# Kernel tuning notes

Hardware: AMD Instinct MI355X
Metric: run time of the kernel (lower is better)

Reference implementation:

```python
import jax, jax.numpy as jnp
import numpy as np

EPS = 1e-6
H = 16  # heads

def rmsnorm(x, w):
    return x * jax.lax.rsqrt(jnp.mean(x * x, axis=-1, keepdims=True) + EPS) * w

def l2norm(x):
    return x * jax.lax.rsqrt(jnp.sum(x * x, axis=-1, keepdims=True) + EPS)

def setup_inputs() -> dict:
    key = jax.random.key(0)
    ks = jax.random.split(key, 12)
    B, S, D, F = 2, 2048, 1024, 4096
    std = 0.02
    inp = {
        'hidden_states': jax.random.normal(ks[0], (B, S, D), jnp.float32),
        'Wq': jax.random.normal(ks[1], (D, D), jnp.float32) * std,
        'Wk': jax.random.normal(ks[2], (D, D), jnp.float32) * std,
        'Wv': jax.random.normal(ks[3], (D, D), jnp.float32) * std,
        'Wb': jax.random.normal(ks[4], (D, H), jnp.float32) * std,
        'Wo': jax.random.normal(ks[5], (D, D), jnp.float32) * std,
        'ln1': jnp.ones((D,), jnp.float32),
        'ln2': jnp.ones((D,), jnp.float32),
        'Wg': jax.random.normal(ks[6], (D, F), jnp.float32) * std,
        'Wu': jax.random.normal(ks[7], (D, F), jnp.float32) * std,
        'Wd': jax.random.normal(ks[8], (F, D), jnp.float32) * std,
    }
    return inp

def delta_rule(q, k, v, beta):
    # q,k: [B,S,H,dk] (l2-normalized), v: [B,S,H,dv], beta: [B,S,H]
    B, S, Hh, dk = q.shape
    dv = v.shape[-1]
    # time-major for scan: [S,B,H,...]
    qt = jnp.moveaxis(q, 1, 0)
    kt = jnp.moveaxis(k, 1, 0)
    vt = jnp.moveaxis(v, 1, 0)
    bt = jnp.moveaxis(beta, 1, 0)

    def step(Sm, inp):
        qi, ki, vi, bi = inp  # [B,H,dk],[B,H,dk],[B,H,dv],[B,H]
        Sk = jnp.einsum('bhkv,bhk->bhv', Sm, ki)          # S^T k
        upd = ki[..., :, None] * (vi - Sk)[..., None, :]  # outer(k, v - S^T k)
        Sm = Sm + bi[..., None, None] * upd
        oi = jnp.einsum('bhkv,bhk->bhv', Sm, qi)
        return Sm, oi

    S0 = jnp.zeros((B, Hh, dk, dv), q.dtype)
    _, out = jax.lax.scan(step, S0, (qt, kt, vt, bt))
    return jnp.moveaxis(out, 0, 1)  # [B,S,H,dv]

def reference(hidden_states, Wq, Wk, Wv, Wb, Wo, ln1, ln2, Wg, Wu, Wd):
    B, S, D = hidden_states.shape
    dk = D // H
    # --- delta-rule attention sub-block ---
    x = rmsnorm(hidden_states, ln1)
    q = l2norm(jax.nn.silu(x @ Wq).reshape(B, S, H, dk))
    k = l2norm(jax.nn.silu(x @ Wk).reshape(B, S, H, dk))
    v = jax.nn.silu(x @ Wv).reshape(B, S, H, dk)
    beta = jax.nn.sigmoid(x @ Wb)  # [B,S,H]
    o = delta_rule(q, k, v, beta).reshape(B, S, D)
    h = hidden_states + o @ Wo
    # --- SwiGLU MLP sub-block ---
    y = rmsnorm(h, ln2)
    h = h + (jax.nn.silu(y @ Wg) * (y @ Wu)) @ Wd
    return h
```

## Files before the change

kernel.cpp:

```cpp
#include <hip/hip_runtime.h>
#include <hip/hip_bf16.h>
#include <stdint.h>

#define BB 2
#define SS 2048
#define DD 1024
#define FF 4096
#define HH 16
#define ROWS (BB*SS)
#define NC 32
#define NQKV 3200

typedef float f32x4 __attribute__((ext_vector_type(4)));
typedef __bf16 bf16x8 __attribute__((ext_vector_type(8)));

typedef __attribute__((address_space(1))) const void* gas1p;
typedef __attribute__((address_space(3))) void* las3p;

__device__ __forceinline__ void gload16(const void* g, void* l) {
    __builtin_amdgcn_global_load_lds((gas1p)g, (las3p)l, 16, 0, 0);
}

__device__ __forceinline__ unsigned short f2bf(float f) {
    unsigned int u = __builtin_bit_cast(unsigned int, f);
    u += 0x7fffu + ((u >> 16) & 1u);
    return (unsigned short)(u >> 16);
}
__device__ __forceinline__ float bf2f(unsigned short s) {
    unsigned int u = ((unsigned int)s) << 16;
    return __builtin_bit_cast(float, u);
}
__device__ __forceinline__ float sigmoidf_(float x) { return 1.f / (1.f + __expf(-x)); }
__device__ __forceinline__ float siluf_(float x)    { return x / (1.f + __expf(-x)); }

__device__ __forceinline__ int swz(int b) { return b ^ (((b >> 7) & 7) << 4); }

__device__ __forceinline__ void tp_body(const float* __restrict__ W,
                                        unsigned short* __restrict__ Wt,
                                        int K, int N, int bx, int by, int tid) {
    __shared__ float tile[32][33];
    int tx = tid & 31, ty = tid >> 5;
    int n0 = bx * 32, k0 = by * 32;
#pragma unroll
    for (int i = 0; i < 4; ++i)
        tile[ty + 8 * i][tx] = W[(size_t)(k0 + ty + 8 * i) * N + n0 + tx];
    __syncthreads();
#pragma unroll
    for (int i = 0; i < 4; ++i)
        Wt[(size_t)(n0 + ty + 8 * i) * K + k0 + tx] = f2bf(tile[tx][ty + 8 * i]);
}

__global__ __launch_bounds__(256) void transpose_cvt(const float* __restrict__ W,
                                                     unsigned short* __restrict__ Wt,
                                                     int K, int N) {
    tp_body(W, Wt, K, N, blockIdx.x, blockIdx.y, threadIdx.x);
}

__global__ __launch_bounds__(256) void transpose_cvt4(const float* W0, const float* W1,
                                                      const float* W2, const float* W3,
                                                      unsigned short* T0, unsigned short* T1,
                                                      unsigned short* T2, unsigned short* T3) {
    const float* W = (blockIdx.z == 0) ? W0 : (blockIdx.z == 1) ? W1 : (blockIdx.z == 2) ? W2 : W3;
    unsigned short* T = (blockIdx.z == 0) ? T0 : (blockIdx.z == 1) ? T1 : (blockIdx.z == 2) ? T2 : T3;
    tp_body(W, T, DD, DD, blockIdx.x, blockIdx.y, threadIdx.x);
}

__global__ __launch_bounds__(256) void transpose_cvt2(const float* W0, const float* W1,
                                                      unsigned short* T0, unsigned short* T1) {
    const float* W = (blockIdx.z == 0) ? W0 : W1;
    unsigned short* T = (blockIdx.z == 0) ? T0 : T1;
    tp_body(W, T, DD, FF, blockIdx.x, blockIdx.y, threadIdx.x);
}

__global__ __launch_bounds__(256) void wbt_kernel(const float* __restrict__ Wb,
                                                  unsigned short* __restrict__ WbT) {
    int idx = blockIdx.x * 256 + threadIdx.x;
    int d = idx >> 4, h = idx & 15;
    WbT[h * DD + d] = f2bf(Wb[idx]);
}

__global__ __launch_bounds__(256) void rmsnorm_bf16_kernel(const float* __restrict__ src,
                                                           const float* __restrict__ w,
                                                           unsigned short* __restrict__ dst) {
    int row = blockIdx.x;
    int tid = threadIdx.x;
    float4 x = ((const float4*)(src + (size_t)row * DD))[tid];
    float ss = x.x * x.x + x.y * x.y + x.z * x.z + x.w * x.w;
#pragma unroll
    for (int m = 1; m < 64; m <<= 1) ss += __shfl_xor(ss, m, 64);
    __shared__ float ws4[4];
    if ((tid & 63) == 0) ws4[tid >> 6] = ss;
    __syncthreads();
    ss = ws4[0] + ws4[1] + ws4[2] + ws4[3];
    float sc = rsqrtf(ss * (1.f / DD) + 1e-6f);
    float4 wv = ((const float4*)w)[tid];
    ushort4 o;
    o.x = f2bf(x.x * sc * wv.x);
    o.y = f2bf(x.y * sc * wv.y);
    o.z = f2bf(x.z * sc * wv.z);
    o.w = f2bf(x.w * sc * wv.w);
    ((ushort4*)(dst + (size_t)row * DD))[tid] = o;
}

#define BM 128
#define BN 128
#define BK 32

template <int EP>
__global__ __launch_bounds__(256) void gemm_bt(const unsigned short* __restrict__ A,
                                               const unsigned short* __restrict__ Bt,
                                               const float* __restrict__ res,
                                               float* __restrict__ cf,
                                               unsigned short* __restrict__ cb,
                                               int M, int N, int K) {
    __shared__ __align__(16) char sA[BM * BK * 2];
    __shared__ __align__(16) char sB[BN * BK * 2];
    int m0 = blockIdx.y * BM, n0 = blockIdx.x * BN;
    int tid = threadIdx.x;
    int lane = tid & 63, wave = tid >> 6;
    int wm = wave >> 1, wn = wave & 1;
    f32x4 acc[4][4] = {};

    for (int k0 = 0; k0 < K; k0 += BK) {
#pragma unroll
        for (int i = 0; i < 2; ++i) {
            int c = wave * 2 + i;
            int row = c * 16 + (lane >> 2);
            int col = (lane & 3) * 8;
            gload16(A  + ((size_t)(m0 + row) * K + k0 + col), (char*)sA + c * 1024);
            gload16(Bt + ((size_t)(n0 + row) * K + k0 + col), (char*)sB + c * 1024);
        }
        __syncthreads();
        bf16x8 af[4], bfr[4];
#pragma unroll
        for (int mi = 0; mi < 4; ++mi) {
            int ar = wm * 64 + mi * 16 + (lane & 15);
            af[mi] = *(const bf16x8*)(sA + ar * 64 + (lane >> 4) * 16);
        }
#pragma unroll
        for (int ni = 0; ni < 4; ++ni) {
            int br = wn * 64 + ni * 16 + (lane & 15);
            bfr[ni] = *(const bf16x8*)(sB + br * 64 + (lane >> 4) * 16);
        }
#pragma unroll
        for (int mi = 0; mi < 4; ++mi)
#pragma unroll
            for (int ni = 0; ni < 4; ++ni)
                acc[mi][ni] = __builtin_amdgcn_mfma_f32_16x16x32_bf16(af[mi], bfr[ni], acc[mi][ni], 0, 0, 0);
        __syncthreads();
    }

    int mbase = m0 + wm * 64 + (lane >> 4) * 4;
    int nbase = n0 + wn * 64 + (lane & 15);
#pragma unroll
    for (int mi = 0; mi < 4; ++mi)
#pragma unroll
        for (int ni = 0; ni < 4; ++ni)
#pragma unroll
            for (int r = 0; r < 4; ++r) {
                int m = mbase + mi * 16 + r;
                int n = nbase + ni * 16;
                float v = acc[mi][ni][r];
                if (EP == 3) {
                    int seg = n >> 10, col = n & 1023;
                    if (seg < 3)
                        cb[(size_t)seg * ROWS * DD + (size_t)m * DD + col] = f2bf(v);
                    else if (col < 16)
                        cf[(size_t)m * HH + col] = sigmoidf_(v);
                } else {
                    if (EP == 1) v += res[(size_t)m * N + n];
                    if (EP == 2) cb[(size_t)m * N + n] = f2bf(v);
                    else         cf[(size_t)m * N + n] = v;
                }
            }
}

__global__ void silu_mul_kernel(unsigned short* __restrict__ g, const unsigned short* __restrict__ u, int n4) {
    int i = blockIdx.x * blockDim.x + threadIdx.x;
    int stride = gridDim.x * blockDim.x;
    ushort4* gp = (ushort4*)g;
    const ushort4* up = (const ushort4*)u;
    for (; i < n4; i += stride) {
        ushort4 gv = gp[i];
        ushort4 uv = up[i];
        ushort4 o;
        o.x = f2bf(siluf_(bf2f(gv.x)) * bf2f(uv.x));
        o.y = f2bf(siluf_(bf2f(gv.y)) * bf2f(uv.y));
        o.z = f2bf(siluf_(bf2f(gv.z)) * bf2f(uv.z));
        o.w = f2bf(siluf_(bf2f(gv.w)) * bf2f(uv.w));
        gp[i] = o;
    }
}


__device__ __forceinline__ bf16x8 ldsfrag(const char* mat, int row, int kt, int lane) {
    return *(const bf16x8*)(mat + swz(row * 128 + kt * 64 + (lane >> 4) * 16));
}

template <bool INIT_P>
__device__ __forceinline__ void mm64(const char* X, const char* Y, const char* P,
                                     f32x4 acc[4], int w, int lane) {
    int g = lane >> 4;
#pragma unroll
    for (int j = 0; j < 4; ++j) {
        if (INIT_P) {
#pragma unroll
            for (int r = 0; r < 4; ++r) {
                int m = 16 * w + g * 4 + r, n = (lane & 15) + 16 * j;
                acc[j][r] = bf2f(*(const unsigned short*)(P + swz(m * 128 + n * 2)));
            }
        } else {
            acc[j] = (f32x4){0.f, 0.f, 0.f, 0.f};
        }
    }
    bf16x8 xs0 = ldsfrag(X, 16 * w + (lane & 15), 0, lane);
    bf16x8 xs1 = ldsfrag(X, 16 * w + (lane & 15), 1, lane);
#pragma unroll
    for (int j = 0; j < 4; ++j) {
        bf16x8 y0 = ldsfrag(Y, 16 * j + (lane & 15), 0, lane);
        bf16x8 y1 = ldsfrag(Y, 16 * j + (lane & 15), 1, lane);
        acc[j] = __builtin_amdgcn_mfma_f32_16x16x32_bf16(xs0, y0, acc[j], 0, 0, 0);
        acc[j] = __builtin_amdgcn_mfma_f32_16x16x32_bf16(xs1, y1, acc[j], 0, 0, 0);
    }
}

__device__ __forceinline__ void wR(char* D, const f32x4 acc[4], int w, int lane, int mode) {
    int g = lane >> 4;
#pragma unroll
    for (int j = 0; j < 4; ++j)
#pragma unroll
        for (int r = 0; r < 4; ++r) {
            int m = 16 * w + g * 4 + r, n = (lane & 15) + 16 * j;
            float v = acc[j][r];
            if (mode >= 1) v = (n < m) ? v : 0.f;
            if (mode == 2) v = ((m == n) ? 1.f : 0.f) - v;
            *(unsigned short*)(D + swz(m * 128 + n * 2)) = f2bf(v);
        }
}

__device__ __forceinline__ void wT(char* D, const f32x4 acc[4], int w, int lane, int mode) {
    int g = lane >> 4;
#pragma unroll
    for (int j = 0; j < 4; ++j) {
        int n = (lane & 15) + 16 * j, m0 = 16 * w + g * 4;
        ushort4 pk;
        pk.x = (mode == 1 && !(n < m0 + 0)) ? (unsigned short)0 : f2bf(acc[j][0]);
        pk.y = (mode == 1 && !(n < m0 + 1)) ? (unsigned short)0 : f2bf(acc[j][1]);
        pk.z = (mode == 1 && !(n < m0 + 2)) ? (unsigned short)0 : f2bf(acc[j][2]);
        pk.w = (mode == 1 && !(n < m0 + 3)) ? (unsigned short)0 : f2bf(acc[j][3]);
        *(ushort4*)(D + swz(n * 128 + m0 * 2)) = pk;
    }
}

__device__ __forceinline__ void load16bf(const unsigned short* p, float* v) {
    uint4 a = *(const uint4*)p, b = *(const uint4*)(p + 8);
    unsigned int u0[8] = {a.x, a.y, a.z, a.w, b.x, b.y, b.z, b.w};
#pragma unroll
    for (int i = 0; i < 8; ++i) {
        v[2 * i]     = bf2f((unsigned short)(u0[i] & 0xffffu));
        v[2 * i + 1] = bf2f((unsigned short)(u0[i] >> 16));
    }
}

__global__ __launch_bounds__(256) void delta_prep_kernel(const unsigned short* __restrict__ qb,
                                                         const unsigned short* __restrict__ kb,
                                                         const unsigned short* __restrict__ vb,
                                                         const float* __restrict__ betab,
                                                         char* __restrict__ chunkbuf) {
    __shared__ __align__(16) char sK[8192], sKb[8192], sKbT[8192], sVbT[8192], sQ[8192];
    __shared__ __align__(16) char mA[8192], mAT[8192], mB2[8192], mBT[8192], mP0[8192], mP1[8192];

    int ci = blockIdx.x;
    int c = ci & 31, h = (ci >> 5) & 15, b = ci >> 9;
    int tid = threadIdx.x;
    int lane = tid & 63, w = tid >> 6;

    char* cbuf = chunkbuf + (size_t)ci * 40960;
    unsigned short* Qg  = (unsigned short*)(cbuf);
    unsigned short* KTg = (unsigned short*)(cbuf + 8192);
    unsigned short* Ag  = (unsigned short*)(cbuf + 16384);
    unsigned short* Wg  = (unsigned short*)(cbuf + 24576);
    unsigned short* U0g = (unsigned short*)(cbuf + 32768);

    {
        int trow = tid >> 2, part = tid & 3, d0 = part * 16;
        size_t rg = (size_t)b * SS + c * 64 + trow;
        float bet = betab[rg * HH + h];
        size_t base = rg * DD + h * 64 + d0;

        float qv[16], kv[16], vv[16];
        load16bf(qb + base, qv);
        load16bf(kb + base, kv);
        load16bf(vb + base, vv);

        float ssq = 0.f, ssk = 0.f;
#pragma unroll
        for (int i = 0; i < 16; ++i) {
            qv[i] = siluf_(qv[i]); ssq += qv[i] * qv[i];
            kv[i] = siluf_(kv[i]); ssk += kv[i] * kv[i];
            vv[i] = siluf_(vv[i]);
        }
        ssq += __shfl_xor(ssq, 1, 64); ssq += __shfl_xor(ssq, 2, 64);
        ssk += __shfl_xor(ssk, 1, 64); ssk += __shfl_xor(ssk, 2, 64);
        float scq = rsqrtf(ssq + 1e-6f), sck = rsqrtf(ssk + 1e-6f);
#pragma unroll
        for (int i = 0; i < 16; ++i) { qv[i] *= scq; kv[i] *= sck; }

#pragma unroll
        for (int m = 0; m < 4; ++m) {
            ushort4 pq, pk_, pkb;
#pragma unroll
            for (int r = 0; r < 4; ++r) {
                ((unsigned short*)&pq)[r]  = f2bf(qv[4 * m + r]);
                ((unsigned short*)&pk_)[r] = f2bf(kv[4 * m + r]);
                ((unsigned short*)&pkb)[r] = f2bf(bet * kv[4 * m + r]);
            }
            int bo = trow * 128 + (d0 + 4 * m) * 2;
            *(ushort4*)(sQ + swz(bo))  = pq;
            *(ushort4*)(sK + swz(bo))  = pk_;
            *(ushort4*)(sKb + swz(bo)) = pkb;
            *(ushort4*)(Qg + trow * 64 + d0 + 4 * m) = pq;
        }
#pragma unroll
        for (int e = 0; e < 16; ++e) {
            int d = d0 + e;
            *(unsigned short*)(sKbT + swz(d * 128 + trow * 2)) = f2bf(bet * kv[e]);
            *(unsigned short*)(sVbT + swz(d * 128 + trow * 2)) = f2bf(bet * vv[e]);
            KTg[d * 64 + trow] = f2bf(kv[e]);
        }
    }
    __syncthreads();

    f32x4 acc[4];
    mm64<false>(sKb, sK, nullptr, acc, w, lane);
    wR(mA, acc, w, lane, 1);
    wT(mAT, acc, w, lane, 1);
    wR(mP0, acc, w, lane, 2);
    __syncthreads();

    char *cX = mA, *cXT = mAT, *nX = mB2, *nXT = mBT, *pc = mP0, *pn = mP1;
#pragma unroll
    for (int s = 0; s < 5; ++s) {
        mm64<false>(cX, cXT, nullptr, acc, w, lane);
        wR(nX, acc, w, lane, 0);
        wT(nXT, acc, w, lane, 0);
        __syncthreads();
        mm64<true>(pc, nXT, pc, acc, w, lane);
        wR(pn, acc, w, lane, 0);
        __syncthreads();
        char* t;
        t = cX; cX = nX; nX = t;
        t = cXT; cXT = nXT; nXT = t;
        t = pc; pc = pn; pn = t;
    }

    int g = lane >> 4;
    mm64<false>(sK, sQ, nullptr, acc, w, lane);
#pragma unroll
    for (int j = 0; j < 4; ++j) {
        int n = (lane & 15) + 16 * j, m0 = 16 * w + g * 4;
        ushort4 pk;
        pk.x = (m0 + 0 <= n) ? f2bf(acc[j][0]) : (unsigned short)0;
        pk.y = (m0 + 1 <= n) ? f2bf(acc[j][1]) : (unsigned short)0;
        pk.z = (m0 + 2 <= n) ? f2bf(acc[j][2]) : (unsigned short)0;
        pk.w = (m0 + 3 <= n) ? f2bf(acc[j][3]) : (unsigned short)0;
        *(ushort4*)(Ag + n * 64 + m0) = pk;
    }
    mm64<false>(sKbT, pc, nullptr, acc, w, lane);
#pragma unroll
    for (int j = 0; j < 4; ++j) {
        int n = (lane & 15) + 16 * j, m0 = 16 * w + g * 4;
        ushort4 pk;
        pk.x = f2bf(acc[j][0]); pk.y = f2bf(acc[j][1]);
        pk.z = f2bf(acc[j][2]); pk.w = f2bf(acc[j][3]);
        *(ushort4*)(Wg + n * 64 + m0) = pk;
    }
    mm64<false>(pc, sVbT, nullptr, acc, w, lane);
#pragma unroll
    for (int j = 0; j < 4; ++j) {
        int n = (lane & 15) + 16 * j, m0 = 16 * w + g * 4;
        ushort4 pk;
        pk.x = f2bf(acc[j][0]); pk.y = f2bf(acc[j][1]);
        pk.z = f2bf(acc[j][2]); pk.w = f2bf(acc[j][3]);
        *(ushort4*)(U0g + n * 64 + m0) = pk;
    }
}

__global__ __launch_bounds__(256) void delta_seq_kernel(const char* __restrict__ chunkbuf,
                                                        unsigned short* __restrict__ ob) {
    __shared__ __align__(16) char stg[2 * 40960 + 8192 + 8192];
    int bh = blockIdx.x;
    int b = bh >> 4, h = bh & 15;
    int tid = threadIdx.x;
    int lane = tid & 63, w = tid >> 6, g = lane >> 4;

    char* UTw = stg + 81920 + w * 2048;
    char* Slw = stg + 90112 + w * 2048;

    f32x4 s_acc[4];
#pragma unroll
    for (int j = 0; j < 4; ++j) s_acc[j] = (f32x4){0.f, 0.f, 0.f, 0.f};
    uint4 z4 = {0, 0, 0, 0};
    *(uint4*)(Slw + lane * 32) = z4;
    *(uint4*)(Slw + lane * 32 + 16) = z4;

    const char* cbase = chunkbuf + (size_t)bh * NC * 40960;
    int lo = (lane * 16) ^ ((lane >> 3) << 4);
    int pw = 10 * w;

    {
        const char* src = cbase;
        char* dst = stg;
#pragma unroll
        for (int p = 0; p < 10; ++p)
            gload16(src + (pw + p) * 1024 + lo, dst + (pw + p) * 1024);
    }

    for (int c = 0; c < NC; ++c) {
        {
            const char* src = cbase + (size_t)((c + 1) & 31) * 40960;
            char* dst = stg + ((c + 1) & 1) * 40960;
#pragma unroll
            for (int p = 0; p < 10; ++p)
                gload16(src + (pw + p) * 1024 + lo, dst + (pw + p) * 1024);
        }
        asm volatile("s_waitcnt vmcnt(10)" ::: "memory");
        __builtin_amdgcn_s_barrier();
        __builtin_amdgcn_sched_barrier(0);

        const char* cur = stg + (c & 1) * 40960;
        const char* Qm = cur, *KTm = cur + 8192, *Am = cur + 16384, *Wm = cur + 24576, *U0m = cur + 32768;

        bf16x8 xs0 = ldsfrag(Slw, lane & 15, 0, lane);
        bf16x8 xs1 = ldsfrag(Slw, lane & 15, 1, lane);

        f32x4 ut[4];
        f32x4 oa[4];
#pragma unroll
        for (int j = 0; j < 4; ++j) { ut[j] = (f32x4){0.f, 0.f, 0.f, 0.f}; oa[j] = (f32x4){0.f, 0.f, 0.f, 0.f}; }
#pragma unroll
        for (int j = 0; j < 4; ++j) {
            bf16x8 y0 = ldsfrag(Wm, 16 * j + (lane & 15), 0, lane);
            bf16x8 y1 = ldsfrag(Wm, 16 * j + (lane & 15), 1, lane);
            ut[j] = __builtin_amdgcn_mfma_f32_16x16x32_bf16(xs0, y0, ut[j], 0, 0, 0);
            ut[j] = __builtin_amdgcn_mfma_f32_16x16x32_bf16(xs1, y1, ut[j], 0, 0, 0);
        }
#pragma unroll
        for (int j = 0; j < 4; ++j) {
            bf16x8 y0 = ldsfrag(Qm, 16 * j + (lane & 15), 0, lane);
            bf16x8 y1 = ldsfrag(Qm, 16 * j + (lane & 15), 1, lane);
            oa[j] = __builtin_amdgcn_mfma_f32_16x16x32_bf16(xs0, y0, oa[j], 0, 0, 0);
            oa[j] = __builtin_amdgcn_mfma_f32_16x16x32_bf16(xs1, y1, oa[j], 0, 0, 0);
        }
#pragma unroll
        for (int j = 0; j < 4; ++j)
#pragma unroll
            for (int r = 0; r < 4; ++r) {
                int m = 16 * w + g * 4 + r;
                int n = (lane & 15) + 16 * j;
                float u0 = bf2f(*(const unsigned short*)(U0m + swz(m * 128 + n * 2)));
                float u = u0 - ut[j][r];
                *(unsigned short*)(UTw + swz((g * 4 + r) * 128 + n * 2)) = f2bf(u);
            }
        bf16x8 us0 = ldsfrag(UTw, lane & 15, 0, lane);
        bf16x8 us1 = ldsfrag(UTw, lane & 15, 1, lane);
#pragma unroll
        for (int j = 0; j < 4; ++j) {
            bf16x8 y0 = ldsfrag(Am, 16 * j + (lane & 15), 0, lane);
            bf16x8 y1 = ldsfrag(Am, 16 * j + (lane & 15), 1, lane);
            oa[j] = __builtin_amdgcn_mfma_f32_16x16x32_bf16(us0, y0, oa[j], 0, 0, 0);
            oa[j] = __builtin_amdgcn_mfma_f32_16x16x32_bf16(us1, y1, oa[j], 0, 0, 0);
        }
#pragma unroll
        for (int j = 0; j < 4; ++j) {
            bf16x8 y0 = ldsfrag(KTm, 16 * j + (lane & 15), 0, lane);
            bf16x8 y1 = ldsfrag(KTm, 16 * j + (lane & 15), 1, lane);
            s_acc[j] = __builtin_amdgcn_mfma_f32_16x16x32_bf16(us0, y0, s_acc[j], 0, 0, 0);
            s_acc[j] = __builtin_amdgcn_mfma_f32_16x16x32_bf16(us1, y1, s_acc[j], 0, 0, 0);
        }
#pragma unroll
        for (int j = 0; j < 4; ++j) {
            int n = (lane & 15) + 16 * j;
            size_t tg = (size_t)b * SS + c * 64 + n;
            int col = h * 64 + 16 * w + g * 4;
            ushort4 pk;
            pk.x = f2bf(oa[j][0]); pk.y = f2bf(oa[j][1]);
            pk.z = f2bf(oa[j][2]); pk.w = f2bf(oa[j][3]);
            *(ushort4*)(ob + tg * DD + col) = pk;
        }
#pragma unroll
        for (int j = 0; j < 4; ++j)
#pragma unroll
            for (int r = 0; r < 4; ++r) {
                int n = (lane & 15) + 16 * j;
                *(unsigned short*)(Slw + swz((g * 4 + r) * 128 + n * 2)) = f2bf(s_acc[j][r]);
            }

        asm volatile("" ::: "memory");
        __builtin_amdgcn_s_barrier();
        __builtin_amdgcn_sched_barrier(0);
    }
}

extern "C" void kernel_launch(void* const* d_in, const int* in_sizes, int n_in,
                              void* d_out, int out_size, void* d_ws, size_t ws_size,
                              hipStream_t stream) {
    const float* hidden = (const float*)d_in[0];
    const float* Wq  = (const float*)d_in[1];
    const float* Wk  = (const float*)d_in[2];
    const float* Wv  = (const float*)d_in[3];
    const float* Wb  = (const float*)d_in[4];
    const float* Wo  = (const float*)d_in[5];
    const float* ln1 = (const float*)d_in[6];
    const float* ln2 = (const float*)d_in[7];
    const float* Wg  = (const float*)d_in[8];
    const float* Wu  = (const float*)d_in[9];
    const float* Wd  = (const float*)d_in[10];
    float* out = (float*)d_out;
    char* ws = (char*)d_ws;

    const size_t MB = 1024 * 1024;
    const size_t KB256 = 262144;
    unsigned short* wq_t = (unsigned short*)(ws + 0 * MB);
    unsigned short* wk_t = (unsigned short*)(ws + 2 * MB);
    unsigned short* wv_t = (unsigned short*)(ws + 4 * MB);
    unsigned short* wbT  = (unsigned short*)(ws + 6 * MB);
    unsigned short* wo_t = (unsigned short*)(ws + 6 * MB + KB256);
    unsigned short* wg_t = (unsigned short*)(ws + 8 * MB + KB256);
    unsigned short* wu_t = (unsigned short*)(ws + 16 * MB + KB256);
    unsigned short* wd_t = (unsigned short*)(ws + 24 * MB + KB256);
    float* hbuf          = (float*)(ws + 32 * MB + KB256);
    unsigned short* yb   = (unsigned short*)(ws + 48 * MB + KB256);
    unsigned short* qb   = (unsigned short*)(ws + 56 * MB + KB256);
    unsigned short* kb   = (unsigned short*)(ws + 64 * MB + KB256);
    unsigned short* vb   = (unsigned short*)(ws + 72 * MB + KB256);
    float* betab         = (float*)(ws + 80 * MB + KB256);
    unsigned short* xb   = (unsigned short*)(ws + 80 * MB + 2 * KB256);
    unsigned short* ob   = xb;
    char* chunkbuf       = ws + 88 * MB + 2 * KB256;
    unsigned short* gb = (unsigned short*)(ws + 56 * MB + KB256);
    unsigned short* ub = (unsigned short*)(ws + 88 * MB + 2 * KB256);

    dim3 blk(256);

    transpose_cvt4<<<dim3(32, 32, 4), blk, 0, stream>>>(Wq, Wk, Wv, Wo, wq_t, wk_t, wv_t, wo_t);
    transpose_cvt2<<<dim3(128, 32, 2), blk, 0, stream>>>(Wg, Wu, wg_t, wu_t);
    transpose_cvt<<<dim3(32, 128), blk, 0, stream>>>(Wd, wd_t, FF, DD);
    wbt_kernel<<<64, blk, 0, stream>>>(Wb, wbT);

    rmsnorm_bf16_kernel<<<ROWS, blk, 0, stream>>>(hidden, ln1, xb);

    gemm_bt<3><<<dim3(NQKV / BN, ROWS / BM), blk, 0, stream>>>(xb, wq_t, nullptr, betab, qb, ROWS, NQKV, DD);

    delta_prep_kernel<<<1024, blk, 0, stream>>>(qb, kb, vb, betab, chunkbuf);
    delta_seq_kernel<<<BB * HH, blk, 0, stream>>>(chunkbuf, ob);

    gemm_bt<1><<<dim3(DD / BN, ROWS / BM), blk, 0, stream>>>(ob, wo_t, hidden, hbuf, nullptr, ROWS, DD, DD);

    rmsnorm_bf16_kernel<<<ROWS, blk, 0, stream>>>(hbuf, ln2, yb);

    gemm_bt<2><<<dim3(FF / BN, ROWS / BM), blk, 0, stream>>>(yb, wg_t, nullptr, nullptr, gb, ROWS, FF, DD);
    gemm_bt<2><<<dim3(FF / BN, ROWS / BM), blk, 0, stream>>>(yb, wu_t, nullptr, nullptr, ub, ROWS, FF, DD);

    silu_mul_kernel<<<4096, blk, 0, stream>>>(gb, ub, ROWS * FF / 4);

    gemm_bt<1><<<dim3(DD / BN, ROWS / BM), blk, 0, stream>>>(gb, wd_t, hbuf, out, nullptr, ROWS, DD, FF);
}
```

Baseline: 555.0 us.

## Fuse gate/up GEMMs with SwiGLU epilogue and double-buffer GEMM with XCD-aware tiling

The Wg and Wu weights are transposed into one interleaved matrix, so a single 256x256-tile GEMM computes gate and up columns side by side and applies silu(g)*u in its epilogue. This removes the separate silu_mul kernel and the write and read-back of both intermediate bf16 buffers. The GEMM is rewritten with BK=64, double-buffered LDS staging, and a block-index remap that groups tiles by XCD for better L2 locality. The large tile uses more LDS and registers, which may lower occupancy.

Result: faster. 464.2 us (-16.4%).

```diff
diff --git a/kernel.cpp b/kernel.cpp
--- a/kernel.cpp
+++ b/kernel.cpp
@@ -65,11 +65,24 @@
     tp_body(W, T, DD, DD, blockIdx.x, blockIdx.y, threadIdx.x);
 }
 
-__global__ __launch_bounds__(256) void transpose_cvt2(const float* W0, const float* W1,
-                                                      unsigned short* T0, unsigned short* T1) {
+__global__ __launch_bounds__(256) void transpose_cvt_gu(const float* W0, const float* W1,
+                                                        unsigned short* Wt) {
     const float* W = (blockIdx.z == 0) ? W0 : W1;
-    unsigned short* T = (blockIdx.z == 0) ? T0 : T1;
-    tp_body(W, T, DD, FF, blockIdx.x, blockIdx.y, threadIdx.x);
+    int isU = blockIdx.z;
+    __shared__ float tile[32][33];
+    int tid = threadIdx.x;
+    int tx = tid & 31, ty = tid >> 5;
+    int n0 = blockIdx.x * 32, k0 = blockIdx.y * 32;
+#pragma unroll
+    for (int i = 0; i < 4; ++i)
+        tile[ty + 8 * i][tx] = W[(size_t)(k0 + ty + 8 * i) * FF + n0 + tx];
+    __syncthreads();
+#pragma unroll
+    for (int i = 0; i < 4; ++i) {
+        int j = n0 + ty + 8 * i;
+        int rint = ((j >> 4) << 5) + (j & 15) + (isU << 4);
+        Wt[(size_t)rint * DD + k0 + tx] = f2bf(tile[tx][ty + 8 * i]);
+    }
 }
 
 __global__ __launch_bounds__(256) void wbt_kernel(const float* __restrict__ Wb,
@@ -102,93 +115,116 @@
     ((ushort4*)(dst + (size_t)row * DD))[tid] = o;
 }
 
-#define BM 128
-#define BN 128
-#define BK 32
-
-template <int EP>
-__global__ __launch_bounds__(256) void gemm_bt(const unsigned short* __restrict__ A,
-                                               const unsigned short* __restrict__ Bt,
-                                               const float* __restrict__ res,
-                                               float* __restrict__ cf,
-                                               unsigned short* __restrict__ cb,
-                                               int M, int N, int K) {
-    __shared__ __align__(16) char sA[BM * BK * 2];
-    __shared__ __align__(16) char sB[BN * BK * 2];
-    int m0 = blockIdx.y * BM, n0 = blockIdx.x * BN;
-    int tid = threadIdx.x;
-    int lane = tid & 63, wave = tid >> 6;
-    int wm = wave >> 1, wn = wave & 1;
-    f32x4 acc[4][4] = {};
-
-    for (int k0 = 0; k0 < K; k0 += BK) {
-#pragma unroll
-        for (int i = 0; i < 2; ++i) {
-            int c = wave * 2 + i;
-            int row = c * 16 + (lane >> 2);
-            int col = (lane & 3) * 8;
-            gload16(A  + ((size_t)(m0 + row) * K + k0 + col), (char*)sA + c * 1024);
-            gload16(Bt + ((size_t)(n0 + row) * K + k0 + col), (char*)sB + c * 1024);
-        }
-        __syncthreads();
-        bf16x8 af[4], bfr[4];
-#pragma unroll
-        for (int mi = 0; mi < 4; ++mi) {
-            int ar = wm * 64 + mi * 16 + (lane & 15);
-            af[mi] = *(const bf16x8*)(sA + ar * 64 + (lane >> 4) * 16);
-        }
-#pragma unroll
-        for (int ni = 0; ni < 4; ++ni) {
-            int br = wn * 64 + ni * 16 + (lane & 15);
-            bfr[ni] = *(const bf16x8*)(sB + br * 64 + (lane >> 4) * 16);
-        }
-#pragma unroll
-        for (int mi = 0; mi < 4; ++mi)
-#pragma unroll
-            for (int ni = 0; ni < 4; ++ni)
-                acc[mi][ni] = __builtin_amdgcn_mfma_f32_16x16x32_bf16(af[mi], bfr[ni], acc[mi][ni], 0, 0, 0);
-        __syncthreads();
-    }
-
-    int mbase = m0 + wm * 64 + (lane >> 4) * 4;
-    int nbase = n0 + wn * 64 + (lane & 15);
-#pragma unroll
-    for (int mi = 0; mi < 4; ++mi)
-#pragma unroll
-        for (int ni = 0; ni < 4; ++ni)
-#pragma unroll
-            for (int r = 0; r < 4; ++r) {
-                int m = mbase + mi * 16 + r;
-                int n = nbase + ni * 16;
-                float v = acc[mi][ni][r];
-                if (EP == 3) {
-                    int seg = n >> 10, col = n & 1023;
-                    if (seg < 3)
-                        cb[(size_t)seg * ROWS * DD + (size_t)m * DD + col] = f2bf(v);
-                    else if (col < 16)
-                        cf[(size_t)m * HH + col] = sigmoidf_(v);
-                } else {
-                    if (EP == 1) v += res[(size_t)m * N + n];
-                    if (EP == 2) cb[(size_t)m * N + n] = f2bf(v);
-                    else         cf[(size_t)m * N + n] = v;
+template <int EP, int BMt, int BNt, int WM, int WN, bool FASTM>
+__global__ __launch_bounds__(WM * WN * 64) void gemm2(const unsigned short* __restrict__ A,
+                                                      const unsigned short* __restrict__ Bt,
+                                                      const float* __restrict__ res,
+                                                      float* __restrict__ cf,
+                                                      unsigned short* __restrict__ cb,
+                                                      int M, int N, int K) {
+    constexpr int NW = WM * WN;
+    constexpr int MI = BMt / (WM * 16);
+    constexpr int NI = BNt / (WN * 16);
+    constexpr int ACH = BMt / 8 / NW;
+    constexpr int BCH = BNt / 8 / NW;
+    constexpr int ABYTES = BMt * 128;
+    constexpr int BBYTES = BNt * 128;
+    __shared__ __align__(16) char lds[2 * (ABYTES + BBYTES)];
+
+    int tid = threadIdx.x, lane = tid & 63, w = tid >> 6;
+    int wm = w / WN, wn = w % WN;
+
+    int gm = M / BMt, gn = N / BNt, nwg = gm * gn;
+    int flat = blockIdx.x;
+    int q = nwg >> 3, r8 = nwg & 7;
+    int xcd = flat & 7, loc = flat >> 3;
+    int sid = (xcd < r8 ? xcd * (q + 1) : r8 * (q + 1) + (xcd - r8) * q) + loc;
+    int midx, nidx;
+    if (FASTM) { midx = sid % gm; nidx = sid / gm; }
+    else       { nidx = sid % gn; midx = sid / gn; }
+    int m0 = midx * BMt, n0 = nidx * BNt;
+
+    auto stage = [&](int buf, int kt) {
+        char* base = (char*)lds + buf * (ABYTES + BBYTES);
+        int row8 = lane >> 3, col = (lane & 7) * 8;
+#pragma unroll
+        for (int i = 0; i < ACH; ++i) {
+            int c = w * ACH + i;
+            gload16(A + ((size_t)(m0 + c * 8 + row8) * K + kt * 64 + col), base + c * 1024);
+        }
+#pragma unroll
+        for (int i = 0; i < BCH; ++i) {
+            int c = w * BCH + i;
+            gload16(Bt + ((size_t)(n0 + c * 8 + row8) * K + kt * 64 + col), base + ABYTES + c * 1024);
+        }
+    };
+
+    f32x4 acc[MI][NI] = {};
+    int nk = K / 64;
+    stage(0, 0);
+    __syncthreads();
+    int cur = 0;
+    for (int kt = 0; kt < nk; ++kt) {
+        if (kt + 1 < nk) stage(cur ^ 1, kt + 1);
+        const char* abuf = (const char*)lds + cur * (ABYTES + BBYTES);
+        const char* bbuf = abuf + ABYTES;
+#pragma unroll
+        for (int kk = 0; kk < 2; ++kk) {
+            bf16x8 afr[MI], bfr[NI];
+#pragma unroll
+            for (int mi = 0; mi < MI; ++mi)
+                afr[mi] = *(const bf16x8*)(abuf + (wm * (MI * 16) + mi * 16 + (lane & 15)) * 128 + kk * 64 + (lane >> 4) * 16);
+#pragma unroll
+            for (int ni = 0; ni < NI; ++ni)
+                bfr[ni] = *(const bf16x8*)(bbuf + (wn * (NI * 16) + ni * 16 + (lane & 15)) * 128 + kk * 64 + (lane >> 4) * 16);
+#pragma unroll
+            for (int mi = 0; mi < MI; ++mi)
+#pragma unroll
+                for (int ni = 0; ni < NI; ++ni)
+                    acc[mi][ni] = __builtin_amdgcn_mfma_f32_16x16x32_bf16(afr[mi], bfr[ni], acc[mi][ni], 0, 0, 0);
+        }
+        if (kt + 1 < nk) {
+            __syncthreads();
+            cur ^= 1;
+        }
+    }
+
+    int mbase = m0 + wm * (MI * 16) + (lane >> 4) * 4;
+    if (EP == 4) {
+        int j0 = (n0 + wn * (NI * 16)) / 2 + (lane & 15);
+#pragma unroll
+        for (int mi = 0; mi < MI; ++mi)
+#pragma unroll
+            for (int p = 0; p < NI / 2; ++p)
+#pragma unroll
+                for (int r = 0; r < 4; ++r) {
+                    int m = mbase + mi * 16 + r;
+                    float gv = acc[mi][2 * p][r], uv = acc[mi][2 * p + 1][r];
+                    cb[(size_t)m * FF + j0 + 16 * p] = f2bf(siluf_(gv) * uv);
                 }
-            }
-}
-
-__global__ void silu_mul_kernel(unsigned short* __restrict__ g, const unsigned short* __restrict__ u, int n4) {
-    int i = blockIdx.x * blockDim.x + threadIdx.x;
-    int stride = gridDim.x * blockDim.x;
-    ushort4* gp = (ushort4*)g;
-    const ushort4* up = (const ushort4*)u;
-    for (; i < n4; i += stride) {
-        ushort4 gv = gp[i];
-        ushort4 uv = up[i];
-        ushort4 o;
-        o.x = f2bf(siluf_(bf2f(gv.x)) * bf2f(uv.x));
-        o.y = f2bf(siluf_(bf2f(gv.y)) * bf2f(uv.y));
-        o.z = f2bf(siluf_(bf2f(gv.z)) * bf2f(uv.z));
-        o.w = f2bf(siluf_(bf2f(gv.w)) * bf2f(uv.w));
-        gp[i] = o;
+    } else {
+        int nbase = n0 + wn * (NI * 16) + (lane & 15);
+#pragma unroll
+        for (int mi = 0; mi < MI; ++mi)
+#pragma unroll
+            for (int ni = 0; ni < NI; ++ni)
+#pragma unroll
+                for (int r = 0; r < 4; ++r) {
+                    int m = mbase + mi * 16 + r;
+                    int n = nbase + ni * 16;
+                    float v = acc[mi][ni][r];
+                    if (EP == 3) {
+                        int seg = n >> 10, col = n & 1023;
+                        if (seg < 3)
+                            cb[(size_t)seg * ROWS * DD + (size_t)m * DD + col] = f2bf(v);
+                        else if (col < 16)
+                            cf[(size_t)m * HH + col] = sigmoidf_(v);
+                    } else {
+                        if (EP == 1) v += res[(size_t)m * N + n];
+                        if (EP == 2) cb[(size_t)m * N + n] = f2bf(v);
+                        else         cf[(size_t)m * N + n] = v;
+                    }
+                }
     }
 }
 
@@ -526,8 +562,7 @@
     unsigned short* wv_t = (unsigned short*)(ws + 4 * MB);
     unsigned short* wbT  = (unsigned short*)(ws + 6 * MB);
     unsigned short* wo_t = (unsigned short*)(ws + 6 * MB + KB256);
-    unsigned short* wg_t = (unsigned short*)(ws + 8 * MB + KB256);
-    unsigned short* wu_t = (unsigned short*)(ws + 16 * MB + KB256);
+    unsigned short* btGU = (unsigned short*)(ws + 8 * MB + KB256);
     unsigned short* wd_t = (unsigned short*)(ws + 24 * MB + KB256);
     float* hbuf          = (float*)(ws + 32 * MB + KB256);
     unsigned short* yb   = (unsigned short*)(ws + 48 * MB + KB256);
@@ -538,31 +573,31 @@
     unsigned short* xb   = (unsigned short*)(ws + 80 * MB + 2 * KB256);
     unsigned short* ob   = xb;
     char* chunkbuf       = ws + 88 * MB + 2 * KB256;
-    unsigned short* gb = (unsigned short*)(ws + 56 * MB + KB256);
-    unsigned short* ub = (unsigned short*)(ws + 88 * MB + 2 * KB256);
+    unsigned short* act  = (unsigned short*)(ws + 56 * MB + KB256);
 
     dim3 blk(256);
 
     transpose_cvt4<<<dim3(32, 32, 4), blk, 0, stream>>>(Wq, Wk, Wv, Wo, wq_t, wk_t, wv_t, wo_t);
-    transpose_cvt2<<<dim3(128, 32, 2), blk, 0, stream>>>(Wg, Wu, wg_t, wu_t);
+    transpose_cvt_gu<<<dim3(128, 32, 2), blk, 0, stream>>>(Wg, Wu, btGU);
     transpose_cvt<<<dim3(32, 128), blk, 0, stream>>>(Wd, wd_t, FF, DD);
     wbt_kernel<<<64, blk, 0, stream>>>(Wb, wbT);
 
     rmsnorm_bf16_kernel<<<ROWS, blk, 0, stream>>>(hidden, ln1, xb);
 
-    gemm_bt<3><<<dim3(NQKV / BN, ROWS / BM), blk, 0, stream>>>(xb, wq_t, nullptr, betab, qb, ROWS, NQKV, DD);
+    gemm2<3, 128, 128, 2, 2, false><<<dim3((NQKV / 128) * (ROWS / 128)), blk, 0, stream>>>(
+        xb, wq_t, nullptr, betab, qb, ROWS, NQKV, DD);
 
     delta_prep_kernel<<<1024, blk, 0, stream>>>(qb, kb, vb, betab, chunkbuf);
     delta_seq_kernel<<<BB * HH, blk, 0, stream>>>(chunkbuf, ob);
 
-    gemm_bt<1><<<dim3(DD / BN, ROWS / BM), blk, 0, stream>>>(ob, wo_t, hidden, hbuf, nullptr, ROWS, DD, DD);
+    gemm2<1, 128, 128, 2, 2, false><<<dim3((DD / 128) * (ROWS / 128)), blk, 0, stream>>>(
+        ob, wo_t, hidden, hbuf, nullptr, ROWS, DD, DD);
 
     rmsnorm_bf16_kernel<<<ROWS, blk, 0, stream>>>(hbuf, ln2, yb);
 
-    gemm_bt<2><<<dim3(FF / BN, ROWS / BM), blk, 0, stream>>>(yb, wg_t, nullptr, nullptr, gb, ROWS, FF, DD);
-    gemm_bt<2><<<dim3(FF / BN, ROWS / BM), blk, 0, stream>>>(yb, wu_t, nullptr, nullptr, ub, ROWS, FF, DD);
-
-    silu_mul_kernel<<<4096, blk, 0, stream>>>(gb, ub, ROWS * FF / 4);
-
-    gemm_bt<1><<<dim3(DD / BN, ROWS / BM), blk, 0, stream>>>(gb, wd_t, hbuf, out, nullptr, ROWS, DD, FF);
-}
+    gemm2<4, 256, 256, 2, 4, true><<<dim3((2 * FF / 256) * (ROWS / 256)), dim3(512), 0, stream>>>(
+        yb, btGU, nullptr, nullptr, act, ROWS, 2 * FF, DD);
+
+    gemm2<1, 128, 128, 2, 2, false><<<dim3((DD / 128) * (ROWS / 128)), blk, 0, stream>>>(
+        act, wd_t, hbuf, out, nullptr, ROWS, DD, FF);
+}
```
